# Optimization experiments

Measured on AMD Instinct MI355X. Metric: run time of the kernel, lower is better.

## Reference

```python
import jax, jax.numpy as jnp
import numpy as np
import math

K = 10      # number of propagation steps
BETA = 2.0  # log-weighting base
N_NODES = 100000
N_EDGES = 1000000
HIDDEN = 64


def setup_inputs() -> dict:
    key = jax.random.key(0)
    k1, k2, k3 = jax.random.split(key, 3)
    feat = jax.random.normal(k1, (N_NODES, HIDDEN), dtype=jnp.float32)
    src = jax.random.randint(k2, (N_EDGES,), 0, N_NODES, dtype=jnp.int64)
    dst = jax.random.randint(k3, (N_EDGES,), 0, N_NODES, dtype=jnp.int64)
    return {"feat": feat, "src": src, "dst": dst}


def reference(feat, src, dst):
    n = feat.shape[0]
    ones_e = jnp.ones(src.shape, dtype=feat.dtype)
    # out-degree of source nodes, in-degree of destination nodes
    out_deg = jax.ops.segment_sum(ones_e, src, num_segments=n)
    in_deg = jax.ops.segment_sum(ones_e, dst, num_segments=n)
    src_norm = jnp.maximum(out_deg, 1.0) ** -0.5  # [N]
    dst_norm = jnp.maximum(in_deg, 1.0) ** -0.5   # [N]

    # log-based combination weights over the K+1 snapshots
    logs = [math.log(BETA + i) for i in range(1, K + 2)]
    denom = sum(logs)
    w = [l / denom for l in logs]

    h = feat
    out = w[0] * feat
    for step in range(K):
        # gather-scale on source side, scatter-sum to destinations, scale on dst side
        m = (h * src_norm[:, None])[src]                      # [E, D]
        h = jax.ops.segment_sum(m, dst, num_segments=n)       # [N, D]
        h = h * dst_norm[:, None]
        out = out + w[step + 1] * h
    return out
```

## Files before the change

### kernel.cpp

```cpp
#include <hip/hip_runtime.h>
#include <hip/hip_bf16.h>
#include <math.h>

#define HIDDEN 64
#define K_STEPS 10
#define SLICES 2
#define SLICE_N 51200
#define SLICE_W (SLICE_N / 4)
#define PADU 4

struct Wts { float v[K_STEPS + 1]; };

typedef float v2f __attribute__((ext_vector_type(2)));

__device__ __forceinline__ float bits2f(unsigned int u) {
    union { unsigned int i; float f; } c; c.i = u; return c.f;
}
__device__ __forceinline__ unsigned short f2bf(float f) {
    union { float f; unsigned int u; } c; c.f = f;
    unsigned int u = c.u;
    return (unsigned short)((u + 0x7FFF + ((u >> 16) & 1)) >> 16);
}
__device__ __forceinline__ void unpack_add(v2f acc[4], uint4 v) {
    v2f t;
    t.x = bits2f(v.x << 16); t.y = bits2f(v.x & 0xFFFF0000u); acc[0] += t;
    t.x = bits2f(v.y << 16); t.y = bits2f(v.y & 0xFFFF0000u); acc[1] += t;
    t.x = bits2f(v.z << 16); t.y = bits2f(v.z & 0xFFFF0000u); acc[2] += t;
    t.x = bits2f(v.w << 16); t.y = bits2f(v.w & 0xFFFF0000u); acc[3] += t;
}

__global__ void detect_kernel(const int* __restrict__ srcw,
                              const unsigned short* __restrict__ featw,
                              int* __restrict__ flags) {
    __shared__ int odd_nonzero;
    __shared__ int exp_in_range;
    if (threadIdx.x == 0) { odd_nonzero = 0; exp_in_range = 0; }
    __syncthreads();
    int w = srcw[2 * threadIdx.x + 1];
    if (w != 0) atomicAdd(&odd_nonzero, 1);
    unsigned short f = featw[2 * threadIdx.x];
    int ex = (f >> 7) & 0xFF;
    if (ex >= 90 && ex <= 135) atomicAdd(&exp_in_range, 1);
    __syncthreads();
    if (threadIdx.x == 0) {
        flags[0] = (odd_nonzero == 0) ? 1 : 0;
        flags[1] = (exp_in_range >= 240) ? 0 : 1;
    }
}

__global__ void hist_kernel(const void* __restrict__ src, const void* __restrict__ dst,
                            const int* __restrict__ flags,
                            unsigned* __restrict__ partials, int E, int chunkE, int nchunks) {
    __shared__ unsigned bins[SLICE_W];
    int cx = blockIdx.x, sy = blockIdx.y, az = blockIdx.z;
    for (int i = threadIdx.x; i < SLICE_W; i += 256) bins[i] = 0;
    __syncthreads();
    const void* arr = az ? dst : src;
    int i64 = flags[0];
    int base = cx * chunkE;
    int lim = min(base + chunkE, E);
    int sliceBase = sy * SLICE_N;
    for (int e = base + threadIdx.x; e < lim; e += 256) {
        int v = i64 ? (int)((const long long*)arr)[e] : ((const int*)arr)[e];
        unsigned local = (unsigned)(v - sliceBase);
        if (local < SLICE_N)
            atomicAdd(&bins[local >> 2], 1u << ((local & 3) * 8));
    }
    __syncthreads();
    unsigned* out = partials + ((size_t)((az * SLICES + sy) * nchunks + cx)) * SLICE_W;
    for (int i = threadIdx.x; i < SLICE_W; i += 256) out[i] = bins[i];
}

__global__ void reduce_kernel(const unsigned* __restrict__ partials,
                              unsigned* __restrict__ chunk_pre,
                              int* __restrict__ out_deg, int* __restrict__ in_deg,
                              int N, int nchunks) {
    int t = blockIdx.x * blockDim.x + threadIdx.x;
    if (t >= 2 * SLICES * SLICE_W) return;
    int a = t / (SLICES * SLICE_W);
    int r = t % (SLICES * SLICE_W);
    int s = r / SLICE_W;
    int lw = r % SLICE_W;
    const unsigned* p = partials + ((size_t)((a * SLICES + s) * nchunks)) * SLICE_W + lw;
    unsigned sum = 0;
    if (a == 1) {
        for (int c = 0; c < nchunks; ++c) {
            chunk_pre[((size_t)(c * SLICES + s)) * SLICE_W + lw] = sum;
            sum += p[(size_t)c * SLICE_W];
        }
    } else {
        for (int c = 0; c < nchunks; ++c) sum += p[(size_t)c * SLICE_W];
    }
    int nodeBase = s * SLICE_N + lw * 4;
    int* deg = a ? in_deg : out_deg;
    #pragma unroll
    for (int k = 0; k < 4; ++k) {
        int n = nodeBase + k;
        if (n < N) deg[n] = (int)((sum >> (k * 8)) & 0xFF);
    }
}

__global__ void norm_kernel(const int* __restrict__ out_deg, const int* __restrict__ in_deg,
                            float* __restrict__ src_norm, float* __restrict__ dst_norm, int N) {
    int n = blockIdx.x * blockDim.x + threadIdx.x;
    if (n < N) {
        src_norm[n] = 1.0f / sqrtf(fmaxf((float)out_deg[n], 1.0f));
        dst_norm[n] = 1.0f / sqrtf(fmaxf((float)in_deg[n], 1.0f));
    }
}

__global__ void scanA_kernel(const int* __restrict__ deg, int* __restrict__ row_ptr,
                             int* __restrict__ block_sums, int N) {
    __shared__ int lds[256];
    int t = threadIdx.x;
    int base = blockIdx.x * 1024 + t * 4;
    int v0 = (base + 0 < N) ? ((deg[base + 0] + (PADU - 1)) & ~(PADU - 1)) : 0;
    int v1 = (base + 1 < N) ? ((deg[base + 1] + (PADU - 1)) & ~(PADU - 1)) : 0;
    int v2 = (base + 2 < N) ? ((deg[base + 2] + (PADU - 1)) & ~(PADU - 1)) : 0;
    int v3 = (base + 3 < N) ? ((deg[base + 3] + (PADU - 1)) & ~(PADU - 1)) : 0;
    int s = v0 + v1 + v2 + v3;
    lds[t] = s;
    __syncthreads();
    for (int off = 1; off < 256; off <<= 1) {
        int x = 0;
        if (t >= off) x = lds[t - off];
        __syncthreads();
        if (t >= off) lds[t] += x;
        __syncthreads();
    }
    int excl = lds[t] - s;
    if (t == 255) block_sums[blockIdx.x] = lds[255];
    if (base + 0 < N) row_ptr[base + 0] = excl;
    if (base + 1 < N) row_ptr[base + 1] = excl + v0;
    if (base + 2 < N) row_ptr[base + 2] = excl + v0 + v1;
    if (base + 3 < N) row_ptr[base + 3] = excl + v0 + v1 + v2;
}

__global__ void scanB_kernel(int* __restrict__ bs, int nb) {
    __shared__ int lds[1024];
    int t = threadIdx.x;
    int v = (t < nb) ? bs[t] : 0;
    lds[t] = v;
    __syncthreads();
    for (int off = 1; off < 1024; off <<= 1) {
        int x = 0;
        if (t >= off) x = lds[t - off];
        __syncthreads();
        if (t >= off) lds[t] += x;
        __syncthreads();
    }
    if (t < nb) bs[t] = lds[t] - v;
    if (t == nb - 1) bs[1024] = lds[t];
}

__global__ void scanC_kernel(const int* __restrict__ block_offs, int* __restrict__ row_ptr,
                             int N) {
    int i = blockIdx.x * blockDim.x + threadIdx.x;
    if (i < N) row_ptr[i] += block_offs[i >> 10];
    if (i == 0) row_ptr[N] = block_offs[1024];
}

__global__ void pad_kernel(const int* __restrict__ in_deg, const int* __restrict__ row_ptr,
                           int* __restrict__ col, int N) {
    int n = blockIdx.x * blockDim.x + threadIdx.x;
    if (n >= N) return;
    int b = row_ptr[n] + in_deg[n];
    int e = row_ptr[n + 1];
    for (int j = b; j < e; ++j) col[j] = N;
}

__global__ void fill_kernel(const void* __restrict__ src, const void* __restrict__ dst,
                            const int* __restrict__ flags,
                            const int* __restrict__ row_ptr,
                            const unsigned* __restrict__ chunk_pre,
                            int* __restrict__ col, int E, int chunkE) {
    __shared__ unsigned bins[SLICE_W];
    int cx = blockIdx.x, sy = blockIdx.y;
    for (int i = threadIdx.x; i < SLICE_W; i += 256) bins[i] = 0;
    __syncthreads();
    int i64 = flags[0];
    int base = cx * chunkE;
    int lim = min(base + chunkE, E);
    int sliceBase = sy * SLICE_N;
    const unsigned* pre_base = chunk_pre + ((size_t)(cx * SLICES + sy)) * SLICE_W;
    for (int e = base + threadIdx.x; e < lim; e += 256) {
        int s, d;
        if (i64) { s = (int)((const long long*)src)[e]; d = (int)((const long long*)dst)[e]; }
        else     { s = ((const int*)src)[e];            d = ((const int*)dst)[e]; }
        unsigned local = (unsigned)(d - sliceBase);
        if (local < SLICE_N) {
            int sh = (local & 3) * 8;
            unsigned old = atomicAdd(&bins[local >> 2], 1u << sh);
            int rank = (int)((old >> sh) & 0xFF);
            int pre = (int)((pre_base[local >> 2] >> sh) & 0xFF);
            col[row_ptr[d] + pre + rank] = s;
        }
    }
}

__global__ void init_kernel(const void* __restrict__ feat_raw,
                            const int* __restrict__ flags,
                            const float* __restrict__ src_norm,
                            uint4* __restrict__ hs8, float4* __restrict__ out_acc4,
                            float w0, int nchunks, int writeAcc) {
    int i = blockIdx.x * blockDim.x + threadIdx.x;
    if (i >= nchunks) return;
    int n = i >> 3;
    int c = i & 7;
    float sn = src_norm[n];
    float f[8];
    if (flags[1]) {
        float4 a = ((const float4*)feat_raw)[i * 2];
        float4 b = ((const float4*)feat_raw)[i * 2 + 1];
        f[0] = a.x; f[1] = a.y; f[2] = a.z; f[3] = a.w;
        f[4] = b.x; f[5] = b.y; f[6] = b.z; f[7] = b.w;
    } else {
        uint4 u = ((const uint4*)feat_raw)[i];
        f[0] = bits2f(u.x << 16); f[1] = bits2f(u.x & 0xFFFF0000u);
        f[2] = bits2f(u.y << 16); f[3] = bits2f(u.y & 0xFFFF0000u);
        f[4] = bits2f(u.z << 16); f[5] = bits2f(u.z & 0xFFFF0000u);
        f[6] = bits2f(u.w << 16); f[7] = bits2f(u.w & 0xFFFF0000u);
    }
    uint4 h;
    h.x = (unsigned int)f2bf(f[0] * sn) | ((unsigned int)f2bf(f[1] * sn) << 16);
    h.y = (unsigned int)f2bf(f[2] * sn) | ((unsigned int)f2bf(f[3] * sn) << 16);
    h.z = (unsigned int)f2bf(f[4] * sn) | ((unsigned int)f2bf(f[5] * sn) << 16);
    h.w = (unsigned int)f2bf(f[6] * sn) | ((unsigned int)f2bf(f[7] * sn) << 16);
    hs8[i] = h;
    if (writeAcc) {
        float4 o0, o1;
        o0.x = w0 * f[0]; o0.y = w0 * f[1]; o0.z = w0 * f[2]; o0.w = w0 * f[3];
        o1.x = w0 * f[4]; o1.y = w0 * f[5]; o1.z = w0 * f[6]; o1.w = w0 * f[7];
        size_t ob = (size_t)n * 16 + c * 2;
        out_acc4[ob] = o0;
        out_acc4[ob + 1] = o1;
    }
}

__global__ void zrow_kernel(uint4* __restrict__ hs_region, int snapN, int nsnap, int N) {
    int i = blockIdx.x * blockDim.x + threadIdx.x;
    int k = i >> 3, r = i & 7;
    if (k < nsnap) {
        uint4 z; z.x = 0u; z.y = 0u; z.z = 0u; z.w = 0u;
        hs_region[(size_t)k * snapN + ((size_t)N << 3) + r] = z;
    }
}

__device__ __forceinline__ void gather_row(const uint4* __restrict__ hs8,
                                           const int* __restrict__ col,
                                           int beg, int end, int fo,
                                           v2f a0[4], v2f a1[4]) {
    int e = beg;
    int nq = (end - beg) >> 2;
    if (nq & 1) {
        int4 c = *(const int4*)(col + e);
        uint4 v0 = hs8[((unsigned)c.x << 3) | fo];
        uint4 v1 = hs8[((unsigned)c.y << 3) | fo];
        uint4 v2 = hs8[((unsigned)c.z << 3) | fo];
        uint4 v3 = hs8[((unsigned)c.w << 3) | fo];
        unpack_add(a0, v0);
        unpack_add(a1, v1);
        unpack_add(a0, v2);
        unpack_add(a1, v3);
        e += 4;
    }
    if (e < end) {
        int4 c0 = *(const int4*)(col + e);
        int4 c1 = *(const int4*)(col + e + 4);
        for (;;) {
            int4 d0 = c0, d1 = c1;
            int ne = e + 8;
            if (ne < end) {
                c0 = *(const int4*)(col + ne);
                c1 = *(const int4*)(col + ne + 4);
            }
            uint4 v0 = hs8[((unsigned)d0.x << 3) | fo];
            uint4 v1 = hs8[((unsigned)d0.y << 3) | fo];
            uint4 v2 = hs8[((unsigned)d0.z << 3) | fo];
            uint4 v3 = hs8[((unsigned)d0.w << 3) | fo];
            uint4 v4 = hs8[((unsigned)d1.x << 3) | fo];
            uint4 v5 = hs8[((unsigned)d1.y << 3) | fo];
            uint4 v6 = hs8[((unsigned)d1.z << 3) | fo];
            uint4 v7 = hs8[((unsigned)d1.w << 3) | fo];
            unpack_add(a0, v0);
            unpack_add(a1, v1);
            unpack_add(a0, v2);
            unpack_add(a1, v3);
            unpack_add(a0, v4);
            unpack_add(a1, v5);
            unpack_add(a0, v6);
            unpack_add(a1, v7);
            e = ne;
            if (e >= end) break;
        }
    }
}

__global__ __launch_bounds__(256) void step_snap(
        const uint4* __restrict__ hs8, const int* __restrict__ row_ptr,
        const int* __restrict__ col, const float* __restrict__ src_norm,
        const float* __restrict__ dst_norm, uint4* __restrict__ hs_next8, int N) {
    int wid = (blockIdx.x * 256 + threadIdx.x) >> 6;
    int nw = (gridDim.x * 256) >> 6;
    int lane = threadIdx.x & 63;
    int grp = lane >> 3, fo = lane & 7;
    for (int nbase = wid * 8; nbase < N; nbase += nw * 8) {
        int node = nbase + grp;
        int beg = 0, end = 0;
        if (node < N) { beg = row_ptr[node]; end = row_ptr[node + 1]; }
        v2f a0[4] = {v2f{0.f,0.f}, v2f{0.f,0.f}, v2f{0.f,0.f}, v2f{0.f,0.f}};
        v2f a1[4] = {v2f{0.f,0.f}, v2f{0.f,0.f}, v2f{0.f,0.f}, v2f{0.f,0.f}};
        if (beg < end) gather_row(hs8, col, beg, end, fo, a0, a1);
        if (node < N) {
            float m = dst_norm[node] * src_norm[node];
            #pragma unroll
            for (int k = 0; k < 4; ++k) a0[k] += a1[k];
            uint4 hn;
            hn.x = (unsigned int)f2bf(a0[0].x * m) | ((unsigned int)f2bf(a0[0].y * m) << 16);
            hn.y = (unsigned int)f2bf(a0[1].x * m) | ((unsigned int)f2bf(a0[1].y * m) << 16);
            hn.z = (unsigned int)f2bf(a0[2].x * m) | ((unsigned int)f2bf(a0[2].y * m) << 16);
            hn.w = (unsigned int)f2bf(a0[3].x * m) | ((unsigned int)f2bf(a0[3].y * m) << 16);
            hs_next8[((unsigned)node << 3) | fo] = hn;
        }
    }
}

template <bool LAST>
__global__ __launch_bounds__(256) void step_acc(
        const uint4* __restrict__ hs8, const int* __restrict__ row_ptr,
        const int* __restrict__ col, const float* __restrict__ src_norm,
        const float* __restrict__ dst_norm, uint4* __restrict__ hs_next8,
        float4* __restrict__ out_acc4, float4* __restrict__ out4, float w, int N) {
    int wid = (blockIdx.x * 256 + threadIdx.x) >> 6;
    int nw = (gridDim.x * 256) >> 6;
    int lane = threadIdx.x & 63;
    int grp = lane >> 3, fo = lane & 7;
    for (int nbase = wid * 8; nbase < N; nbase += nw * 8) {
        int node = nbase + grp;
        int beg = 0, end = 0;
        if (node < N) { beg = row_ptr[node]; end = row_ptr[node + 1]; }
        v2f a0[4] = {v2f{0.f,0.f}, v2f{0.f,0.f}, v2f{0.f,0.f}, v2f{0.f,0.f}};
        v2f a1[4] = {v2f{0.f,0.f}, v2f{0.f,0.f}, v2f{0.f,0.f}, v2f{0.f,0.f}};
        if (beg < end) gather_row(hs8, col, beg, end, fo, a0, a1);
        if (node < N) {
            #pragma unroll
            for (int k = 0; k < 4; ++k) a0[k] += a1[k];
            float dn = dst_norm[node];
            float h0 = a0[0].x * dn, h1 = a0[0].y * dn, h2 = a0[1].x * dn, h3 = a0[1].y * dn;
            float h4 = a0[2].x * dn, h5 = a0[2].y * dn, h6 = a0[3].x * dn, h7 = a0[3].y * dn;
            size_t ob = (size_t)node * 16 + fo * 2;
            float4 o0 = out_acc4[ob];
            float4 o1 = out_acc4[ob + 1];
            o0.x += w * h0; o0.y += w * h1; o0.z += w * h2; o0.w += w * h3;
            o1.x += w * h4; o1.y += w * h5; o1.z += w * h6; o1.w += w * h7;
            if (LAST) {
                out4[ob] = o0;
                out4[ob + 1] = o1;
            } else {
                out_acc4[ob] = o0;
                out_acc4[ob + 1] = o1;
                float sn = src_norm[node];
                uint4 hn;
                hn.x = (unsigned int)f2bf(h0 * sn) | ((unsigned int)f2bf(h1 * sn) << 16);
                hn.y = (unsigned int)f2bf(h2 * sn) | ((unsigned int)f2bf(h3 * sn) << 16);
                hn.z = (unsigned int)f2bf(h4 * sn) | ((unsigned int)f2bf(h5 * sn) << 16);
                hn.w = (unsigned int)f2bf(h6 * sn) | ((unsigned int)f2bf(h7 * sn) << 16);
                hs_next8[((unsigned)node << 3) | fo] = hn;
            }
        }
    }
}

__global__ void combine_kernel(const void* __restrict__ feat_raw,
                               const int* __restrict__ flags,
                               const int* __restrict__ out_deg,
                               const uint4* __restrict__ hs_base,
                               float4* __restrict__ out4,
                               Wts wts, int snapN, int nchunks) {
    int i = blockIdx.x * blockDim.x + threadIdx.x;
    if (i >= nchunks) return;
    int n = i >> 3;
    float inv = sqrtf(fmaxf((float)out_deg[n], 1.0f));
    float acc[8];
    if (flags[1]) {
        float4 a = ((const float4*)feat_raw)[i * 2];
        float4 b = ((const float4*)feat_raw)[i * 2 + 1];
        acc[0] = a.x; acc[1] = a.y; acc[2] = a.z; acc[3] = a.w;
        acc[4] = b.x; acc[5] = b.y; acc[6] = b.z; acc[7] = b.w;
    } else {
        uint4 u = ((const uint4*)feat_raw)[i];
        acc[0] = bits2f(u.x << 16); acc[1] = bits2f(u.x & 0xFFFF0000u);
        acc[2] = bits2f(u.y << 16); acc[3] = bits2f(u.y & 0xFFFF0000u);
        acc[4] = bits2f(u.z << 16); acc[5] = bits2f(u.z & 0xFFFF0000u);
        acc[6] = bits2f(u.w << 16); acc[7] = bits2f(u.w & 0xFFFF0000u);
    }
    float w0 = wts.v[0];
    #pragma unroll
    for (int j = 0; j < 8; ++j) acc[j] *= w0;
    #pragma unroll
    for (int k = 1; k <= K_STEPS; ++k) {
        uint4 u = hs_base[(size_t)k * snapN + i];
        float s = wts.v[k] * inv;
        acc[0] += s * bits2f(u.x << 16); acc[1] += s * bits2f(u.x & 0xFFFF0000u);
        acc[2] += s * bits2f(u.y << 16); acc[3] += s * bits2f(u.y & 0xFFFF0000u);
        acc[4] += s * bits2f(u.z << 16); acc[5] += s * bits2f(u.z & 0xFFFF0000u);
        acc[6] += s * bits2f(u.w << 16); acc[7] += s * bits2f(u.w & 0xFFFF0000u);
    }
    float4 o0 = {acc[0], acc[1], acc[2], acc[3]};
    float4 o1 = {acc[4], acc[5], acc[6], acc[7]};
    out4[i * 2] = o0;
    out4[i * 2 + 1] = o1;
}

extern "C" void kernel_launch(void* const* d_in, const int* in_sizes, int n_in,
                              void* d_out, int out_size, void* d_ws, size_t ws_size,
                              hipStream_t stream) {
    const void* feat_raw = d_in[0];
    const void* src_raw = d_in[1];
    const void* dst_raw = d_in[2];
    float4* out4 = (float4*)d_out;

    const int N = in_sizes[0] / HIDDEN;
    const int E = (in_sizes[1] > 1500000) ? in_sizes[1] / 2 : in_sizes[1];
    const int nchunks = N * 8;
    const int snapN = nchunks + 8;
    const int Ecap = E + (PADU - 1) * N + 16;

    auto align256 = [](size_t b) { return (b + 255) & ~(size_t)255; };
    size_t base_bytes = align256(2 * sizeof(int))
                      + align256((size_t)N * sizeof(int))
                      + align256((size_t)N * sizeof(int))
                      + align256((size_t)(N + 1) * sizeof(int))
                      + align256(1025 * sizeof(int))
                      + align256((size_t)Ecap * sizeof(int))
                      + align256((size_t)N * sizeof(float))
                      + align256((size_t)N * sizeof(float));
    auto hist_bytes = [&](int C) {
        return align256((size_t)2 * SLICES * C * SLICE_W * sizeof(unsigned))
             + align256((size_t)C * SLICES * SLICE_W * sizeof(unsigned));
    };
    size_t snap_bytes = align256((size_t)(K_STEPS + 1) * snapN * sizeof(uint4));
    size_t acc_bytes  = align256((size_t)2 * snapN * sizeof(uint4))
                      + align256((size_t)N * 16 * sizeof(float4));

    int CH;
    int snapMode;
    if      (ws_size >= base_bytes + hist_bytes(64) + snap_bytes) { CH = 64; snapMode = 1; }
    else if (ws_size >= base_bytes + hist_bytes(32) + snap_bytes) { CH = 32; snapMode = 1; }
    else if (ws_size >= base_bytes + hist_bytes(64) + acc_bytes)  { CH = 64; snapMode = 0; }
    else                                                          { CH = 32; snapMode = 0; }
    const int chunkE = (E + CH - 1) / CH;

    char* p = (char*)d_ws;
    auto alloc = [&](size_t bytes) {
        char* r = p;
        p += (bytes + 255) & ~(size_t)255;
        return r;
    };
    int* flags = (int*)alloc(2 * sizeof(int));
    int* out_deg = (int*)alloc((size_t)N * sizeof(int));
    int* in_deg = (int*)alloc((size_t)N * sizeof(int));
    int* row_ptr = (int*)alloc((size_t)(N + 1) * sizeof(int));
    int* block_sums = (int*)alloc(1025 * sizeof(int));
    int* col = (int*)alloc((size_t)Ecap * sizeof(int));
    float* src_norm = (float*)alloc((size_t)N * sizeof(float));
    float* dst_norm = (float*)alloc((size_t)N * sizeof(float));
    unsigned* partials = (unsigned*)alloc((size_t)2 * SLICES * CH * SLICE_W * sizeof(unsigned));
    unsigned* chunk_pre = (unsigned*)alloc((size_t)CH * SLICES * SLICE_W * sizeof(unsigned));
    uint4* hs_region;
    float4* out_acc = nullptr;
    if (snapMode) {
        hs_region = (uint4*)alloc((size_t)(K_STEPS + 1) * snapN * sizeof(uint4));
    } else {
        hs_region = (uint4*)alloc((size_t)2 * snapN * sizeof(uint4));
        out_acc = (float4*)alloc((size_t)N * 16 * sizeof(float4));
    }

    double logs[K_STEPS + 1];
    double denom = 0.0;
    for (int i = 0; i < K_STEPS + 1; ++i) {
        logs[i] = log(2.0 + (double)(i + 1));
        denom += logs[i];
    }
    Wts wts;
    for (int i = 0; i < K_STEPS + 1; ++i) wts.v[i] = (float)(logs[i] / denom);

    detect_kernel<<<1, 256, 0, stream>>>((const int*)src_raw,
                                         (const unsigned short*)feat_raw, flags);
    hist_kernel<<<dim3(CH, SLICES, 2), 256, 0, stream>>>(src_raw, dst_raw, flags,
                                                         partials, E, chunkE, CH);
    reduce_kernel<<<(2 * SLICES * SLICE_W + 255) / 256, 256, 0, stream>>>(
        partials, chunk_pre, out_deg, in_deg, N, CH);
    norm_kernel<<<(N + 255) / 256, 256, 0, stream>>>(out_deg, in_deg, src_norm, dst_norm, N);

    int nb = (N + 1023) / 1024;
    scanA_kernel<<<nb, 256, 0, stream>>>(in_deg, row_ptr, block_sums, N);
    scanB_kernel<<<1, 1024, 0, stream>>>(block_sums, nb);
    scanC_kernel<<<(N + 255) / 256, 256, 0, stream>>>(block_sums, row_ptr, N);
    pad_kernel<<<(N + 255) / 256, 256, 0, stream>>>(in_deg, row_ptr, col, N);
    fill_kernel<<<dim3(CH, SLICES), 256, 0, stream>>>(src_raw, dst_raw, flags,
                                                      row_ptr, chunk_pre, col, E, chunkE);

    init_kernel<<<(nchunks + 255) / 256, 256, 0, stream>>>(
        feat_raw, flags, src_norm, hs_region, out_acc, wts.v[0], nchunks, snapMode ? 0 : 1);
    zrow_kernel<<<1, 128, 0, stream>>>(hs_region, snapN, snapMode ? (K_STEPS + 1) : 2, N);

    const int step_blocks = (((N + 7) / 8) + 3) / 4;
    if (snapMode) {
        for (int step = 0; step < K_STEPS; ++step) {
            const uint4* cur = hs_region + (size_t)step * snapN;
            uint4* nxt = hs_region + (size_t)(step + 1) * snapN;
            step_snap<<<step_blocks, 256, 0, stream>>>(cur, row_ptr, col, src_norm,
                                                       dst_norm, nxt, N);
        }
        combine_kernel<<<(nchunks + 255) / 256, 256, 0, stream>>>(
            feat_raw, flags, out_deg, hs_region, out4, wts, snapN, nchunks);
    } else {
        uint4* cur = hs_region;
        uint4* nxt = hs_region + snapN;
        for (int step = 0; step < K_STEPS; ++step) {
            if (step == K_STEPS - 1) {
                step_acc<true><<<step_blocks, 256, 0, stream>>>(
                    cur, row_ptr, col, src_norm, dst_norm, nxt, out_acc, out4,
                    wts.v[step + 1], N);
            } else {
                step_acc<false><<<step_blocks, 256, 0, stream>>>(
                    cur, row_ptr, col, src_norm, dst_norm, nxt, out_acc, out4,
                    wts.v[step + 1], N);
            }
            uint4* t = cur; cur = nxt; nxt = t;
        }
    }
}
```

Baseline: 404.4 us.

## Record per-edge ranks in histogram pass and replace fill with parallel scatter

The histogram kernel now saves each edge's local rank (the old byte count returned by the shared-memory atomic) for the destination array into a per-edge byte buffer. The CSR fill pass no longer reruns shared-memory atomics per chunk and slice; a flat grid-stride scatter kernel reads the saved rank plus the chunk prefix and writes col directly. Chunks become fixed power-of-two sizes (8192 edges), so there are many more histogram blocks and partials. This adds an E-byte buffer and a larger partials/reduce workload in exchange for a much more parallel fill step. Byte-packed counters still assume no more than 255 hits per node within one chunk.

```diff
diff --git a/kernel.cpp b/kernel.cpp
--- a/kernel.cpp
+++ b/kernel.cpp
@@ -50,7 +50,9 @@
 
 __global__ void hist_kernel(const void* __restrict__ src, const void* __restrict__ dst,
                             const int* __restrict__ flags,
-                            unsigned* __restrict__ partials, int E, int chunkE, int nchunks) {
+                            unsigned* __restrict__ partials,
+                            unsigned char* __restrict__ rank,
+                            int E, int chunkE, int nchunks) {
     __shared__ unsigned bins[SLICE_W];
     int cx = blockIdx.x, sy = blockIdx.y, az = blockIdx.z;
     for (int i = threadIdx.x; i < SLICE_W; i += 256) bins[i] = 0;
@@ -63,8 +65,11 @@
     for (int e = base + threadIdx.x; e < lim; e += 256) {
         int v = i64 ? (int)((const long long*)arr)[e] : ((const int*)arr)[e];
         unsigned local = (unsigned)(v - sliceBase);
-        if (local < SLICE_N)
-            atomicAdd(&bins[local >> 2], 1u << ((local & 3) * 8));
+        if (local < SLICE_N) {
+            int sh = (local & 3) * 8;
+            unsigned old = atomicAdd(&bins[local >> 2], 1u << sh);
+            if (az) rank[e] = (unsigned char)((old >> sh) & 0xFF);
+        }
     }
     __syncthreads();
     unsigned* out = partials + ((size_t)((az * SLICES + sy) * nchunks + cx)) * SLICE_W;
@@ -169,32 +174,24 @@
     for (int j = b; j < e; ++j) col[j] = N;
 }
 
-__global__ void fill_kernel(const void* __restrict__ src, const void* __restrict__ dst,
-                            const int* __restrict__ flags,
-                            const int* __restrict__ row_ptr,
-                            const unsigned* __restrict__ chunk_pre,
-                            int* __restrict__ col, int E, int chunkE) {
-    __shared__ unsigned bins[SLICE_W];
-    int cx = blockIdx.x, sy = blockIdx.y;
-    for (int i = threadIdx.x; i < SLICE_W; i += 256) bins[i] = 0;
-    __syncthreads();
+__global__ void scatter_kernel(const void* __restrict__ src, const void* __restrict__ dst,
+                               const int* __restrict__ flags,
+                               const int* __restrict__ row_ptr,
+                               const unsigned* __restrict__ chunk_pre,
+                               const unsigned char* __restrict__ rank,
+                               int* __restrict__ col, int E, int chunkShift) {
     int i64 = flags[0];
-    int base = cx * chunkE;
-    int lim = min(base + chunkE, E);
-    int sliceBase = sy * SLICE_N;
-    const unsigned* pre_base = chunk_pre + ((size_t)(cx * SLICES + sy)) * SLICE_W;
-    for (int e = base + threadIdx.x; e < lim; e += 256) {
+    int stride = gridDim.x * blockDim.x;
+    for (int e = blockIdx.x * blockDim.x + threadIdx.x; e < E; e += stride) {
         int s, d;
         if (i64) { s = (int)((const long long*)src)[e]; d = (int)((const long long*)dst)[e]; }
         else     { s = ((const int*)src)[e];            d = ((const int*)dst)[e]; }
-        unsigned local = (unsigned)(d - sliceBase);
-        if (local < SLICE_N) {
-            int sh = (local & 3) * 8;
-            unsigned old = atomicAdd(&bins[local >> 2], 1u << sh);
-            int rank = (int)((old >> sh) & 0xFF);
-            int pre = (int)((pre_base[local >> 2] >> sh) & 0xFF);
-            col[row_ptr[d] + pre + rank] = s;
-        }
+        int c = e >> chunkShift;
+        int si = (d >= SLICE_N) ? 1 : 0;
+        unsigned local = (unsigned)d - si * SLICE_N;
+        unsigned prew = chunk_pre[((size_t)(c * SLICES + si)) * SLICE_W + (local >> 2)];
+        int pre = (int)((prew >> ((local & 3) * 8)) & 0xFF);
+        col[row_ptr[d] + pre + (int)rank[e]] = s;
     }
 }
 
@@ -434,7 +431,8 @@
                       + align256(1025 * sizeof(int))
                       + align256((size_t)Ecap * sizeof(int))
                       + align256((size_t)N * sizeof(float))
-                      + align256((size_t)N * sizeof(float));
+                      + align256((size_t)N * sizeof(float))
+                      + align256((size_t)E);
     auto hist_bytes = [&](int C) {
         return align256((size_t)2 * SLICES * C * SLICE_W * sizeof(unsigned))
              + align256((size_t)C * SLICES * SLICE_W * sizeof(unsigned));
@@ -443,13 +441,25 @@
     size_t acc_bytes  = align256((size_t)2 * snapN * sizeof(uint4))
                       + align256((size_t)N * 16 * sizeof(float4));
 
-    int CH;
+    int chunkShift = 13;
+    int CHc = (E + (1 << chunkShift) - 1) >> chunkShift;
     int snapMode;
-    if      (ws_size >= base_bytes + hist_bytes(64) + snap_bytes) { CH = 64; snapMode = 1; }
-    else if (ws_size >= base_bytes + hist_bytes(32) + snap_bytes) { CH = 32; snapMode = 1; }
-    else if (ws_size >= base_bytes + hist_bytes(64) + acc_bytes)  { CH = 64; snapMode = 0; }
-    else                                                          { CH = 32; snapMode = 0; }
-    const int chunkE = (E + CH - 1) / CH;
+    if (ws_size >= base_bytes + hist_bytes(CHc) + snap_bytes) {
+        snapMode = 1;
+    } else {
+        chunkShift = 14;
+        CHc = (E + (1 << chunkShift) - 1) >> chunkShift;
+        if (ws_size >= base_bytes + hist_bytes(CHc) + snap_bytes) {
+            snapMode = 1;
+        } else if (ws_size >= base_bytes + hist_bytes(CHc) + acc_bytes) {
+            snapMode = 0;
+        } else {
+            chunkShift = 15;
+            CHc = (E + (1 << chunkShift) - 1) >> chunkShift;
+            snapMode = 0;
+        }
+    }
+    const int chunkE = 1 << chunkShift;
 
     char* p = (char*)d_ws;
     auto alloc = [&](size_t bytes) {
@@ -465,8 +475,9 @@
     int* col = (int*)alloc((size_t)Ecap * sizeof(int));
     float* src_norm = (float*)alloc((size_t)N * sizeof(float));
     float* dst_norm = (float*)alloc((size_t)N * sizeof(float));
-    unsigned* partials = (unsigned*)alloc((size_t)2 * SLICES * CH * SLICE_W * sizeof(unsigned));
-    unsigned* chunk_pre = (unsigned*)alloc((size_t)CH * SLICES * SLICE_W * sizeof(unsigned));
+    unsigned char* rank = (unsigned char*)alloc((size_t)E);
+    unsigned* partials = (unsigned*)alloc((size_t)2 * SLICES * CHc * SLICE_W * sizeof(unsigned));
+    unsigned* chunk_pre = (unsigned*)alloc((size_t)CHc * SLICES * SLICE_W * sizeof(unsigned));
     uint4* hs_region;
     float4* out_acc = nullptr;
     if (snapMode) {
@@ -487,10 +498,10 @@
 
     detect_kernel<<<1, 256, 0, stream>>>((const int*)src_raw,
                                          (const unsigned short*)feat_raw, flags);
-    hist_kernel<<<dim3(CH, SLICES, 2), 256, 0, stream>>>(src_raw, dst_raw, flags,
-                                                         partials, E, chunkE, CH);
+    hist_kernel<<<dim3(CHc, SLICES, 2), 256, 0, stream>>>(src_raw, dst_raw, flags,
+                                                          partials, rank, E, chunkE, CHc);
     reduce_kernel<<<(2 * SLICES * SLICE_W + 255) / 256, 256, 0, stream>>>(
-        partials, chunk_pre, out_deg, in_deg, N, CH);
+        partials, chunk_pre, out_deg, in_deg, N, CHc);
     norm_kernel<<<(N + 255) / 256, 256, 0, stream>>>(out_deg, in_deg, src_norm, dst_norm, N);
 
     int nb = (N + 1023) / 1024;
@@ -498,8 +509,8 @@
     scanB_kernel<<<1, 1024, 0, stream>>>(block_sums, nb);
     scanC_kernel<<<(N + 255) / 256, 256, 0, stream>>>(block_sums, row_ptr, N);
     pad_kernel<<<(N + 255) / 256, 256, 0, stream>>>(in_deg, row_ptr, col, N);
-    fill_kernel<<<dim3(CH, SLICES), 256, 0, stream>>>(src_raw, dst_raw, flags,
-                                                      row_ptr, chunk_pre, col, E, chunkE);
+    scatter_kernel<<<min(2048, (E + 255) / 256), 256, 0, stream>>>(
+        src_raw, dst_raw, flags, row_ptr, chunk_pre, rank, col, E, chunkShift);
 
     init_kernel<<<(nchunks + 255) / 256, 256, 0, stream>>>(
         feat_raw, flags, src_norm, hs_region, out_acc, wts.v[0], nchunks, snapMode ? 0 : 1);
```

Result: faster. 390.3 us (-3.5%).
